# Performance work log

Measured on AMD Instinct MI355X. Metric: run time of the kernel, lower is better.

The kernel has to match this reference:

```python
import jax, jax.numpy as jnp
import numpy as np

EPS = 1e-5


def ste_sign(x):
    # Binarize(x) = sign(x) with straight-through identity gradient (torch .data trick)
    return x + jax.lax.stop_gradient(jnp.sign(x) - x)


def conv3x3(x, w):
    # NCHW 3x3 conv, stride 1, zero padding 1 (== ZeroPad2d(1) + 9 shifted views)
    return jax.lax.conv_general_dilated(x, w, (1, 1), [(1, 1), (1, 1)],
                                        dimension_numbers=('NCHW', 'OIHW', 'NCHW'))


def bconv(x, w):
    # Sum of 9 (or 18/36 channel-chunked) shifted binarized 1x1 convs == one binarized 3x3 conv.
    # sign(0)=0 on the zero padding, identical to padding the binarized input.
    return conv3x3(ste_sign(x), ste_sign(w))


def maxpool2(x):
    return jax.lax.reduce_window(x, -jnp.inf, jax.lax.max, (1, 1, 2, 2), (1, 1, 2, 2), 'VALID')


def bn(x, g, b):
    # eval-mode BatchNorm with fresh running stats (mean=0, var=1, eps=1e-5)
    scale = g * jax.lax.rsqrt(jnp.asarray(1.0 + EPS, x.dtype))
    shape = (1, -1) + (1,) * (x.ndim - 2)
    return x * scale.reshape(shape) + b.reshape(shape)


def htanh(x):
    return jnp.clip(x, -1.0, 1.0)


def blinear(x, w, b):
    # BinarizeLinear: in_features != 784 so both input and weight are binarized
    return ste_sign(x) @ ste_sign(w).T + b


def setup_inputs() -> dict:
    key = jax.random.key(0)
    ks = iter(jax.random.split(key, 48))

    def rn(shape, scale=0.05):
        return jax.random.normal(next(ks), shape, dtype=jnp.float32) * scale

    inp = {"x": jax.random.normal(next(ks), (128, 3, 32, 32), dtype=jnp.float32)}
    inp.update(
        w1=rn((128, 3, 3, 3)), c1b=rn((128,)),
        w2=rn((128, 128, 3, 3)),
        w3=rn((256, 128, 3, 3)),
        w4=rn((256, 256, 3, 3)),
        w5=rn((512, 256, 3, 3)),
        w6=rn((512, 512, 3, 3)),
        fw1=rn((1024, 8192)), fb1=rn((1024,)),
        fw2=rn((1024, 1024)), fb2=rn((1024,)),
        fw3=rn((10, 1024)), fb3=rn((10,)),
    )
    for name, c in [("1", 128), ("2", 128), ("3", 256), ("4", 256), ("5", 512), ("6", 512),
                    ("f1", 1024), ("f2", 1024), ("f3", 10)]:
        inp["g" + name] = jax.random.normal(next(ks), (c,), dtype=jnp.float32) * 0.1 + 1.0
        inp["bt" + name] = rn((c,))
    return inp


def reference(x, w1, c1b, w2, w3, w4, w5, w6,
              fw1, fb1, fw2, fb2, fw3, fb3,
              g1, bt1, g2, bt2, g3, bt3, g4, bt4, g5, bt5, g6, bt6,
              gf1, btf1, gf2, btf2, gf3, btf3):
    # block 1: first conv keeps the 3-channel input real, binarizes only the weight
    h = conv3x3(x, ste_sign(w1)) + c1b.reshape(1, -1, 1, 1)
    h = htanh(bn(h, g1, bt1))
    # block 2: 9 shifted binarized 1x1 convs (128->128) -> pool -> BN -> hardtanh
    h = htanh(bn(maxpool2(bconv(h, w2)), g2, bt2))
    # block 3: 9 convs 128->256
    h = htanh(bn(bconv(h, w3), g3, bt3))
    h = htanh(bn(maxpool2(bconv(h, w4)), g4, bt4))
    h = htanh(bn(bconv(h, w5), g5, bt5))
    h = htanh(bn(maxpool2(bconv(h, w6)), g6, bt6))
    h = h.reshape(h.shape[0], -1)  # [B, 512*4*4]
    h = htanh(bn(blinear(h, fw1, fb1), gf1, btf1))
    h = htanh(bn(blinear(h, fw2, fb2), gf2, btf2))
    h = bn(blinear(h, fw3, fb3), gf3, btf3)
    return jax.nn.log_softmax(h, axis=-1)
```

## Files before the change

### kernel.cpp

```cpp
#include <hip/hip_runtime.h>
#include <hip/hip_bf16.h>

using u32 = unsigned int;
using u64 = unsigned long long;
using s8  = signed char;
typedef int i32x4  __attribute__((ext_vector_type(4)));
typedef int i32x16 __attribute__((ext_vector_type(16)));

__device__ __forceinline__ s8 tsign(float t){
  return (t > 0.f) ? (s8)1 : ((t < 0.f) ? (s8)-1 : (s8)0);
}
__device__ __forceinline__ float bn_ts(float z, float sc, float b){
  return __fadd_rn(__fmul_rn(z, sc), b);
}

__global__ void scales_k(const float* g1, const float* g2, const float* g3,
                         const float* g4, const float* g5, const float* g6,
                         const float* gf1, const float* gf2, const float* gf3,
                         float* sc){
  int i = blockIdx.x*256 + threadIdx.x;
  const float rs = __fdiv_rn(1.0f, __fsqrt_rn((float)(1.0 + 1e-5)));
  float v;
  if      (i < 128)  v = g1[i];
  else if (i < 256)  v = g2[i-128];
  else if (i < 512)  v = g3[i-256];
  else if (i < 768)  v = g4[i-512];
  else if (i < 1280) v = g5[i-768];
  else if (i < 1792) v = g6[i-1280];
  else if (i < 2816) v = gf1[i-1792];
  else if (i < 3840) v = gf2[i-2816];
  else if (i < 3850) v = gf3[i-3840];
  else return;
  sc[i] = __fmul_rn(v, rs);
}

__global__ __launch_bounds__(256) void pack_wfrag_all_k(
    const float* __restrict__ w2, const float* __restrict__ w3,
    const float* __restrict__ w4, const float* __restrict__ w5,
    const float* __restrict__ w6,
    s8* __restrict__ wf2, s8* __restrict__ wf3, s8* __restrict__ wf4,
    s8* __restrict__ wf5, s8* __restrict__ wf6){
  int b = blockIdx.x;
  const float* w; s8* wf; int CIN, COUT, co;
  if      (b < 128) { w=w2; wf=wf2; CIN=128; COUT=128; co=b; }
  else if (b < 384) { w=w3; wf=wf3; CIN=128; COUT=256; co=b-128; }
  else if (b < 640) { w=w4; wf=wf4; CIN=256; COUT=256; co=b-384; }
  else if (b < 1152){ w=w5; wf=wf5; CIN=256; COUT=512; co=b-640; }
  else              { w=w6; wf=wf6; CIN=512; COUT=512; co=b-1152; }
  __shared__ s8 sb[4608];
  int nf = CIN*9;
  const float* wb = w + (size_t)co*nf;
  for (int i = threadIdx.x; i < nf; i += 256){
    float v = wb[i];
    sb[i] = (v > 0.f) ? (s8)1 : ((v < 0.f) ? (s8)-1 : (s8)0);
  }
  __syncthreads();
  int KK = CIN >> 5, CG = COUT >> 5;
  int cg = co >> 5, llo = co & 31;
  for (int i = threadIdx.x; i < nf; i += 256){
    int tap = i / CIN, k = i - tap*CIN;
    s8 v = sb[k*9 + tap];
    size_t dst = ((((size_t)tap*KK + (k>>5))*CG + cg)*64
                  + (llo + ((k>>4)&1)*32))*16 + (k&15);
    wf[dst] = v;
  }
}

__global__ void pack_w1_k(const float* __restrict__ w1, u32* __restrict__ wp1){
  int lane = threadIdx.x;
  bool hz = false;
  for (int h = 0; h < 2; h++){
    int co = h*64 + lane;
    u32 a = 0, s = 0, ctlw = 0;
    for (int tap = 0; tap < 9; tap++){
      float v0 = w1[(co*3 + 0)*9 + tap];
      float v1 = w1[(co*3 + 1)*9 + tap];
      float v2 = w1[(co*3 + 2)*9 + tap];
      int b0 = tap*3;
      a |= ((v0 != 0.f) ? 1u : 0u) << b0;     s |= ((v0 > 0.f) ? 1u : 0u) << b0;
      a |= ((v1 != 0.f) ? 1u : 0u) << (b0+1); s |= ((v1 > 0.f) ? 1u : 0u) << (b0+1);
      a |= ((v2 != 0.f) ? 1u : 0u) << (b0+2); s |= ((v2 > 0.f) ? 1u : 0u) << (b0+2);
      hz |= (v0 == 0.f) || (v1 == 0.f) || (v2 == 0.f);
      u32 f = (((v0 > 0.f) == (v1 > 0.f)) ? 1u : 0u)
            | ((v0 < 0.f) ? 2u : 0u)
            | ((v2 < 0.f) ? 4u : 0u);
      ctlw |= f << b0;
    }
    wp1[co*2]   = a;
    wp1[co*2+1] = s;
    wp1[256 + co] = ctlw;
  }
  u64 m = __ballot(hz);
  if (lane == 0) wp1[384] = (m != 0ull) ? 1u : 0u;
}

__global__ __launch_bounds__(256) void pack_fcB_k(const float* __restrict__ wa,
    const float* __restrict__ wb3, u32* __restrict__ wpa, u32* __restrict__ wpb){
  int b = blockIdx.x;
  const float* w; u32* wp; int COUT, co;
  if (b < 1024){ w = wa; wp = wpa; COUT = 1024; co = b; }
  else         { w = wb3; wp = wpb; COUT = 10;  co = b-1024; }
  __shared__ unsigned char sb[1024];
  const float* wbp = w + (size_t)co*1024;
  for (int i = threadIdx.x; i < 1024; i += 256){
    float v = wbp[i];
    sb[i] = (unsigned char)(((v != 0.f) ? 2u : 0u) | ((v > 0.f) ? 1u : 0u));
  }
  __syncthreads();
  for (int kw = threadIdx.x; kw < 32; kw += 256){
    u32 a = 0, s = 0;
    for (int j = 0; j < 32; j++){
      unsigned char bch = sb[kw*32 + j];
      a |= (u32)(bch >> 1) << j;
      s |= (u32)(bch & 1u) << j;
    }
    size_t o = ((size_t)kw*COUT + co)*2;
    wp[o] = a; wp[o+1] = s;
  }
}

__global__ __launch_bounds__(256) void pack_fc1_2k(const float* __restrict__ w,
    u32* __restrict__ wp){
  int co = blockIdx.x;
  __shared__ unsigned char sb[8192];
  const float* wb = w + (size_t)co*8192;
  for (int i = threadIdx.x; i < 8192; i += 256){
    float v = wb[i];
    sb[i] = (unsigned char)(((v != 0.f) ? 2u : 0u) | ((v > 0.f) ? 1u : 0u));
  }
  __syncthreads();
  int kw = threadIdx.x;
  int px = kw >> 4, cw = kw & 15;
  u32 a = 0, s = 0;
  for (int j = 0; j < 32; j++){
    unsigned char bch = sb[(cw*32 + j)*16 + px];
    a |= (u32)(bch >> 1) << j;
    s |= (u32)(bch & 1u) << j;
  }
  size_t o = ((size_t)kw*1024 + co)*2;
  wp[o] = a; wp[o+1] = s;
}

__global__ __launch_bounds__(256) void conv1_k(
    const float* __restrict__ x, const u32* __restrict__ wp1,
    const float* __restrict__ c1b,
    const float* __restrict__ sc1, const float* __restrict__ bt1,
    s8* __restrict__ s1){
  int tid = threadIdx.x, lane = tid & 63, wv = tid >> 6;
  int wid = blockIdx.x*4 + wv;
  int coh = wid & 1;
  int chunk = (wid >> 1) & 15;
  int n = wid >> 5;
  int py = lane >> 5, px = lane & 31;
  int y = chunk*2 + py;
  const float* xb = x + (size_t)n*3*1024;

  float xv[3][9];
  #pragma unroll
  for (int ci = 0; ci < 3; ci++)
    #pragma unroll
    for (int tap = 0; tap < 9; tap++){
      int yy = y + tap/3 - 1, xx = px + tap%3 - 1;
      bool ok = ((unsigned)yy < 32u) && ((unsigned)xx < 32u);
      xv[ci][tap] = ok ? xb[(ci*32 + yy)*32 + xx] : 0.f;
    }
  float pc0[9], pc1[9];
  #pragma unroll
  for (int tap = 0; tap < 9; tap++){
    pc0[tap] = __fadd_rn(xv[0][tap], xv[1][tap]);
    pc1[tap] = __fadd_rn(xv[0][tap], -xv[1][tap]);
  }

  size_t pixbase = (((size_t)n*1024) + y*32 + px)*128 + coh*64;
  bool fallback = (wp1[384] != 0u);

  if (!fallback){
    for (int co4 = 0; co4 < 64; co4 += 4){
      u32 outw = 0;
      #pragma unroll
      for (int j = 0; j < 4; j++){
        int co = coh*64 + co4 + j;
        u32 ctlw = wp1[256 + co];
        float acc = 0.f;
        #pragma unroll
        for (int tap = 0; tap < 9; tap++){
          u32 f = ctlw >> (3*tap);
          float s01 = (f & 1u) ? pc0[tap] : pc1[tap];
          s01 = __uint_as_float(__float_as_uint(s01) ^ ((f & 2u) << 30));
          float t2 = __uint_as_float(__float_as_uint(xv[2][tap]) ^ ((f & 4u) << 29));
          acc = __fadd_rn(acc, __fadd_rn(s01, t2));
        }
        float v = __fadd_rn(acc, c1b[co]);
        float t = bn_ts(v, sc1[co], bt1[co]);
        outw |= ((u32)(unsigned char)tsign(t)) << (8*j);
      }
      *reinterpret_cast<u32*>(&s1[pixbase + co4]) = outw;
    }
  } else {
    for (int co4 = 0; co4 < 64; co4 += 4){
      u32 outw = 0;
      #pragma unroll
      for (int j = 0; j < 4; j++){
        int co = coh*64 + co4 + j;
        u32 wA = wp1[co*2], wS = wp1[co*2+1];
        float acc = 0.f;
        #pragma unroll
        for (int tap = 0; tap < 9; tap++){
          float pt = 0.f;
          #pragma unroll
          for (int ci = 0; ci < 3; ci++){
            int bit = tap*3 + ci;
            float sg = ((wA >> bit) & 1u) ? (((wS >> bit) & 1u) ? 1.f : -1.f) : 0.f;
            pt = __fadd_rn(pt, __fmul_rn(sg, xv[ci][tap]));
          }
          acc = __fadd_rn(acc, pt);
        }
        float v = __fadd_rn(acc, c1b[co]);
        float t = bn_ts(v, sc1[co], bt1[co]);
        outw |= ((u32)(unsigned char)tsign(t)) << (8*j);
      }
      *reinterpret_cast<u32*>(&s1[pixbase + co4]) = outw;
    }
  }
}

template<int CIN, int COUT, int H, int W, int POOL, int BITOUT>
__global__ __launch_bounds__(256) void bconv_m(
    const s8* __restrict__ A, const s8* __restrict__ WF,
    const float* __restrict__ sc, const float* __restrict__ bt,
    s8* __restrict__ O, u32* __restrict__ OB){
  constexpr int KK = CIN/32, CG = COUT/32, CGB = 2;
  constexpr int XT = (W >= 16) ? 16 : 8;
  constexpr int YT = 32 / XT;
  constexpr int TPR = W / XT;
  constexpr int TROWS = H / YT;
  constexpr int HO = POOL ? H/2 : H, WO = POOL ? W/2 : W;
  int tid = threadIdx.x, lane = tid & 63, wv = tid >> 6;
  int wid = blockIdx.x*4 + wv;
  int cb = wid % (CG/CGB); int mt = wid / (CG/CGB);
  int tx = mt % TPR; int r0 = mt / TPR;
  int ty = r0 % TROWS; int n = r0 / TROWS;
  int y0 = ty*YT, x0 = tx*XT;
  int p = lane & 31;
  int py = p / XT, px = p % XT;
  int y = y0 + py, x = x0 + px;
  int kh = lane >> 5;
  const s8* An = A + (size_t)n*H*W*CIN;

  i32x16 acc0 = {0,0,0,0,0,0,0,0,0,0,0,0,0,0,0,0};
  i32x16 acc1 = {0,0,0,0,0,0,0,0,0,0,0,0,0,0,0,0};

  #pragma unroll
  for (int tap = 0; tap < 9; tap++){
    int dy = tap/3 - 1, dx = tap%3 - 1;
    int sy = y + dy, sx = x + dx;
    bool ok = ((unsigned)sy < (unsigned)H) && ((unsigned)sx < (unsigned)W);
    const s8* ap = An + ((size_t)sy*W + sx)*CIN + kh*16;
    const s8* wp = WF + (((size_t)tap*KK)*CG + (size_t)cb*CGB)*1024 + lane*16;
    #pragma unroll
    for (int kk = 0; kk < KK; kk++){
      i32x4 av = {0,0,0,0};
      if (ok) av = *reinterpret_cast<const i32x4*>(ap + kk*32);
      const s8* wk = wp + (size_t)kk*CG*1024;
      i32x4 b0 = *reinterpret_cast<const i32x4*>(wk);
      i32x4 b1 = *reinterpret_cast<const i32x4*>(wk + 1024);
      acc0 = __builtin_amdgcn_mfma_i32_32x32x32_i8(av, b0, acc0, 0, 0, 0);
      acc1 = __builtin_amdgcn_mfma_i32_32x32x32_i8(av, b1, acc1, 0, 0, 0);
    }
  }

  #pragma unroll
  for (int cgb = 0; cgb < CGB; cgb++){
    i32x16 acc = cgb ? acc1 : acc0;
    int co = (cb*CGB + cgb)*32 + (lane & 31);
    float ss = sc[co], bb = bt[co];
    if (POOL){
      constexpr int RY = (XT == 16) ? 8 : 4;
      #pragma unroll
      for (int q = 0; q < 4; q++){
        int rr = (q&1)*2 + (q>>1)*((XT == 16) ? 4 : 8);
        int z = max(max(acc[rr], acc[rr+1]), max(acc[rr+RY], acc[rr+RY+1]));
        float t = bn_ts((float)z, ss, bb);
        if (!BITOUT){
          int pb = (rr&3) + 8*(rr>>2) + 4*kh;
          int yy = y0 + pb/XT, xx2 = x0 + pb%XT;
          int oy = yy >> 1, ox = xx2 >> 1;
          O[(((size_t)n*HO + oy)*WO + ox)*COUT + co] = tsign(t);
        } else {
          u64 mP = __ballot(t > 0.f);
          u64 mN = __ballot(t < 0.f);
          if (lane == 0){
            u64 mA = mP | mN;
            int cw = cb*CGB + cgb;
            int pb0 = (rr&3) + 8*(rr>>2);
            int yy0 = y0 + pb0/XT, xx0 = x0 + pb0%XT;
            int p0 = (yy0>>1)*4 + (xx0>>1);
            int pb1 = pb0 + 4;
            int yy1 = y0 + pb1/XT, xx1 = x0 + pb1%XT;
            int p1 = (yy1>>1)*4 + (xx1>>1);
            size_t o0 = ((size_t)n*256 + p0*16 + cw)*2;
            size_t o1 = ((size_t)n*256 + p1*16 + cw)*2;
            OB[o0]   = (u32)mA;       OB[o0+1] = (u32)mP;
            OB[o1]   = (u32)(mA>>32); OB[o1+1] = (u32)(mP>>32);
          }
        }
      }
    } else {
      #pragma unroll
      for (int rr = 0; rr < 16; rr++){
        int pb = (rr&3) + 8*(rr>>2) + 4*kh;
        int yy = y0 + pb/XT, xx2 = x0 + pb%XT;
        float t = bn_ts((float)acc[rr], ss, bb);
        O[(((size_t)n*H + yy)*W + xx2)*COUT + co] = tsign(t);
      }
    }
  }
}

template<int KW>
__global__ __launch_bounds__(256) void fcb_k(
    const u32* __restrict__ A, const u32* __restrict__ Wp,
    const float* __restrict__ fb,
    const float* __restrict__ sc, const float* __restrict__ bt,
    u32* __restrict__ Op){
  int tid = threadIdx.x; int lane = tid & 63; int wv = tid >> 6;
  int wid = blockIdx.x*4 + wv;
  int og = wid & 15; int n = wid >> 4;
  int o = og*64 + lane;
  const uint2* a = reinterpret_cast<const uint2*>(&A[(size_t)n*KW*2]);
  int z = 0;
  #pragma unroll 8
  for (int kw = 0; kw < KW; kw++){
    uint2 av = a[kw];
    uint2 wv_ = reinterpret_cast<const uint2*>(Wp)[kw*1024 + o];
    u32 v = av.x & wv_.x;
    u32 d = v & (av.y ^ wv_.y);
    z += __popc(v) - 2*__popc(d);
  }
  float vv = __fadd_rn((float)z, fb[o]);
  float t = bn_ts(vv, sc[o], bt[o]);
  u64 mP = __ballot(t > 0.f);
  u64 mN = __ballot(t < 0.f);
  if (lane == 0){
    int ob = (n*32 + og*2)*2;
    Op[ob]   = (u32)(mP | mN);
    Op[ob+1] = (u32)mP;
    Op[ob+2] = (u32)((mP | mN) >> 32);
    Op[ob+3] = (u32)(mP >> 32);
  }
}

__global__ void fc3_k(const u32* __restrict__ A, const u32* __restrict__ Wp,
                      const float* __restrict__ fb,
                      const float* __restrict__ sc,
                      const float* __restrict__ bt,
                      float* __restrict__ out){
  int n = blockIdx.x; int lane = threadIdx.x;
  __shared__ double ls[10];
  double t = 0.0;
  if (lane < 10){
    const uint2* a = reinterpret_cast<const uint2*>(&A[(size_t)n*32*2]);
    int z = 0;
    for (int kw = 0; kw < 32; kw++){
      uint2 av = a[kw];
      uint2 wv_ = reinterpret_cast<const uint2*>(Wp)[kw*10 + lane];
      u32 v = av.x & wv_.x;
      u32 d = v & (av.y ^ wv_.y);
      z += __popc(v) - 2*__popc(d);
    }
    float vv = __fadd_rn((float)z, fb[lane]);
    float tf = bn_ts(vv, sc[lane], bt[lane]);
    t = (double)tf;
    ls[lane] = t;
  }
  __syncthreads();
  if (lane < 10){
    double m = -1e300;
    for (int j = 0; j < 10; j++) m = fmax(m, ls[j]);
    double sum = 0.0;
    for (int j = 0; j < 10; j++) sum += exp(ls[j] - m);
    double r = t - m - log(sum);
    out[n*10 + lane] = (float)r;
  }
}

extern "C" void kernel_launch(void* const* d_in, const int* in_sizes, int n_in,
                              void* d_out, int out_size, void* d_ws, size_t ws_size,
                              hipStream_t stream){
  auto f = [&](int i){ return (const float*)d_in[i]; };
  const float *x  = f(0),  *w1 = f(1),  *c1b = f(2),
    *w2 = f(3),  *w3 = f(4),  *w4 = f(5),  *w5 = f(6),  *w6 = f(7),
    *fw1 = f(8), *fb1 = f(9), *fw2 = f(10), *fb2 = f(11),
    *fw3 = f(12), *fb3 = f(13),
    *g1 = f(14), *bt1 = f(15), *g2 = f(16), *bt2 = f(17),
    *g3 = f(18), *bt3 = f(19), *g4 = f(20), *bt4 = f(21),
    *g5 = f(22), *bt5 = f(23), *g6 = f(24), *bt6 = f(25),
    *gf1 = f(26), *btf1 = f(27), *gf2 = f(28), *btf2 = f(29),
    *gf3 = f(30), *btf3 = f(31);

  char* base = (char*)d_ws;
  size_t off = 0;
  auto alloc = [&](size_t bytes){ char* p = base + off; off += (bytes + 255) & ~(size_t)255; return p; };
  s8* poolA = (s8*)alloc(128ull*32*32*128);
  s8* poolB = (s8*)alloc(128ull*16*16*128);
  s8 *s1 = poolA, *s3 = poolA, *s5 = poolA;
  s8 *s2 = poolB, *s4 = poolB;
  s8 *wf2 = (s8*)alloc(9ull*128*128), *wf3 = (s8*)alloc(9ull*128*256),
     *wf4 = (s8*)alloc(9ull*256*256), *wf5 = (s8*)alloc(9ull*256*512),
     *wf6 = (s8*)alloc(9ull*512*512);
  u32 *wp1  = (u32*)alloc(385*4);
  float* scb = (float*)alloc(3850*4);
  u32 *fw1p = (u32*)alloc(2ull*256*1024*4), *fw2p = (u32*)alloc(2ull*32*1024*4),
      *fw3p = (u32*)alloc(2ull*32*10*4);
  u32 *s6p  = (u32*)alloc(2ull*128*256*4);
  u32 *sf1  = (u32*)alloc(2ull*128*32*4), *sf2 = (u32*)alloc(2ull*128*32*4);

  float *sc1 = scb, *sc2 = scb+128, *sc3 = scb+256, *sc4 = scb+512,
        *sc5 = scb+768, *sc6 = scb+1280, *scf1 = scb+1792, *scf2 = scb+2816,
        *scf3 = scb+3840;

  scales_k<<<16, 256, 0, stream>>>(g1,g2,g3,g4,g5,g6,gf1,gf2,gf3, scb);
  pack_w1_k<<<1, 64, 0, stream>>>(w1, wp1);
  pack_wfrag_all_k<<<1664, 256, 0, stream>>>(w2,w3,w4,w5,w6, wf2,wf3,wf4,wf5,wf6);
  pack_fc1_2k<<<1024, 256, 0, stream>>>(fw1, fw1p);
  pack_fcB_k<<<1034, 256, 0, stream>>>(fw2, fw3, fw2p, fw3p);

  conv1_k<<<1024, 256, 0, stream>>>(x, wp1, c1b, sc1, bt1, s1);
  bconv_m<128,128,32,32,1,0><<<2048, 256, 0, stream>>>(s1, wf2, sc2, bt2, s2, nullptr);
  bconv_m<128,256,16,16,0,0><<<1024, 256, 0, stream>>>(s2, wf3, sc3, bt3, s3, nullptr);
  bconv_m<256,256,16,16,1,0><<<1024, 256, 0, stream>>>(s3, wf4, sc4, bt4, s4, nullptr);
  bconv_m<256,512, 8, 8,0,0><<< 512, 256, 0, stream>>>(s4, wf5, sc5, bt5, s5, nullptr);
  bconv_m<512,512, 8, 8,1,1><<< 512, 256, 0, stream>>>(s5, wf6, sc6, bt6, nullptr, s6p);
  fcb_k<256><<<(128*16)/4, 256, 0, stream>>>(s6p, fw1p, fb1, scf1, btf1, sf1);
  fcb_k<32><<<(128*16)/4,  256, 0, stream>>>(sf1, fw2p, fb2, scf2, btf2, sf2);
  fc3_k<<<128, 64, 0, stream>>>(sf2, fw3p, fb3, scf3, btf3, (float*)d_out);
}
```

Baseline: 352.2 us.

## Widen bconv wave tile to four output groups and split conv1 channels finer

Each bconv wave now computes 128 output channels (four MFMA accumulators) per 32-pixel tile instead of 64, so every activation load is reused across twice as many output channels. The work mapping is also reordered so consecutive waves share a channel group and walk over pixel tiles, improving weight locality, and grid sizes are halved to match. conv1 splits output channels into four quarters per pixel, doubling its grid, and stages results in registers so it writes two 16-byte stores instead of many 4-byte ones. The wider tile raises register pressure and gives fewer waves for small layers, which may lower occupancy.

```diff
diff --git a/kernel.cpp b/kernel.cpp
--- a/kernel.cpp
+++ b/kernel.cpp
@@ -148,9 +148,9 @@
     s8* __restrict__ s1){
   int tid = threadIdx.x, lane = tid & 63, wv = tid >> 6;
   int wid = blockIdx.x*4 + wv;
-  int coh = wid & 1;
-  int chunk = (wid >> 1) & 15;
-  int n = wid >> 5;
+  int coh = wid & 3;
+  int chunk = (wid >> 2) & 15;
+  int n = wid >> 6;
   int py = lane >> 5, px = lane & 31;
   int y = chunk*2 + py;
   const float* xb = x + (size_t)n*3*1024;
@@ -171,15 +171,17 @@
     pc1[tap] = __fadd_rn(xv[0][tap], -xv[1][tap]);
   }
 
-  size_t pixbase = (((size_t)n*1024) + y*32 + px)*128 + coh*64;
+  size_t pixbase = (((size_t)n*1024) + y*32 + px)*128 + coh*32;
   bool fallback = (wp1[384] != 0u);
+  u32 ow[8];
 
   if (!fallback){
-    for (int co4 = 0; co4 < 64; co4 += 4){
+    #pragma unroll
+    for (int co4 = 0; co4 < 32; co4 += 4){
       u32 outw = 0;
       #pragma unroll
       for (int j = 0; j < 4; j++){
-        int co = coh*64 + co4 + j;
+        int co = coh*32 + co4 + j;
         u32 ctlw = wp1[256 + co];
         float acc = 0.f;
         #pragma unroll
@@ -194,14 +196,15 @@
         float t = bn_ts(v, sc1[co], bt1[co]);
         outw |= ((u32)(unsigned char)tsign(t)) << (8*j);
       }
-      *reinterpret_cast<u32*>(&s1[pixbase + co4]) = outw;
+      ow[co4/4] = outw;
     }
   } else {
-    for (int co4 = 0; co4 < 64; co4 += 4){
+    #pragma unroll
+    for (int co4 = 0; co4 < 32; co4 += 4){
       u32 outw = 0;
       #pragma unroll
       for (int j = 0; j < 4; j++){
-        int co = coh*64 + co4 + j;
+        int co = coh*32 + co4 + j;
         u32 wA = wp1[co*2], wS = wp1[co*2+1];
         float acc = 0.f;
         #pragma unroll
@@ -219,9 +222,13 @@
         float t = bn_ts(v, sc1[co], bt1[co]);
         outw |= ((u32)(unsigned char)tsign(t)) << (8*j);
       }
-      *reinterpret_cast<u32*>(&s1[pixbase + co4]) = outw;
-    }
-  }
+      ow[co4/4] = outw;
+    }
+  }
+  uint4 st0 = { ow[0], ow[1], ow[2], ow[3] };
+  uint4 st1 = { ow[4], ow[5], ow[6], ow[7] };
+  *reinterpret_cast<uint4*>(&s1[pixbase])      = st0;
+  *reinterpret_cast<uint4*>(&s1[pixbase + 16]) = st1;
 }
 
 template<int CIN, int COUT, int H, int W, int POOL, int BITOUT>
@@ -229,15 +236,17 @@
     const s8* __restrict__ A, const s8* __restrict__ WF,
     const float* __restrict__ sc, const float* __restrict__ bt,
     s8* __restrict__ O, u32* __restrict__ OB){
-  constexpr int KK = CIN/32, CG = COUT/32, CGB = 2;
+  constexpr int KK = CIN/32, CG = COUT/32;
   constexpr int XT = (W >= 16) ? 16 : 8;
   constexpr int YT = 32 / XT;
   constexpr int TPR = W / XT;
   constexpr int TROWS = H / YT;
+  constexpr int NMT = 128*TROWS*TPR;
   constexpr int HO = POOL ? H/2 : H, WO = POOL ? W/2 : W;
+  constexpr int RY = (XT == 16) ? 8 : 4;
   int tid = threadIdx.x, lane = tid & 63, wv = tid >> 6;
   int wid = blockIdx.x*4 + wv;
-  int cb = wid % (CG/CGB); int mt = wid / (CG/CGB);
+  int mt = wid % NMT; int cb = wid / NMT;
   int tx = mt % TPR; int r0 = mt / TPR;
   int ty = r0 % TROWS; int n = r0 / TROWS;
   int y0 = ty*YT, x0 = tx*XT;
@@ -248,7 +257,7 @@
   const s8* An = A + (size_t)n*H*W*CIN;
 
   i32x16 acc0 = {0,0,0,0,0,0,0,0,0,0,0,0,0,0,0,0};
-  i32x16 acc1 = {0,0,0,0,0,0,0,0,0,0,0,0,0,0,0,0};
+  i32x16 acc1 = acc0, acc2 = acc0, acc3 = acc0;
 
   #pragma unroll
   for (int tap = 0; tap < 9; tap++){
@@ -256,7 +265,7 @@
     int sy = y + dy, sx = x + dx;
     bool ok = ((unsigned)sy < (unsigned)H) && ((unsigned)sx < (unsigned)W);
     const s8* ap = An + ((size_t)sy*W + sx)*CIN + kh*16;
-    const s8* wp = WF + (((size_t)tap*KK)*CG + (size_t)cb*CGB)*1024 + lane*16;
+    const s8* wp = WF + (((size_t)tap*KK)*CG + (size_t)cb*4)*1024 + lane*16;
     #pragma unroll
     for (int kk = 0; kk < KK; kk++){
       i32x4 av = {0,0,0,0};
@@ -264,18 +273,19 @@
       const s8* wk = wp + (size_t)kk*CG*1024;
       i32x4 b0 = *reinterpret_cast<const i32x4*>(wk);
       i32x4 b1 = *reinterpret_cast<const i32x4*>(wk + 1024);
+      i32x4 b2 = *reinterpret_cast<const i32x4*>(wk + 2048);
+      i32x4 b3 = *reinterpret_cast<const i32x4*>(wk + 3072);
       acc0 = __builtin_amdgcn_mfma_i32_32x32x32_i8(av, b0, acc0, 0, 0, 0);
       acc1 = __builtin_amdgcn_mfma_i32_32x32x32_i8(av, b1, acc1, 0, 0, 0);
-    }
-  }
-
-  #pragma unroll
-  for (int cgb = 0; cgb < CGB; cgb++){
-    i32x16 acc = cgb ? acc1 : acc0;
-    int co = (cb*CGB + cgb)*32 + (lane & 31);
+      acc2 = __builtin_amdgcn_mfma_i32_32x32x32_i8(av, b2, acc2, 0, 0, 0);
+      acc3 = __builtin_amdgcn_mfma_i32_32x32x32_i8(av, b3, acc3, 0, 0, 0);
+    }
+  }
+
+  auto epi = [&](const i32x16& acc, int cgb){
+    int co = (cb*4 + cgb)*32 + (lane & 31);
     float ss = sc[co], bb = bt[co];
     if (POOL){
-      constexpr int RY = (XT == 16) ? 8 : 4;
       #pragma unroll
       for (int q = 0; q < 4; q++){
         int rr = (q&1)*2 + (q>>1)*((XT == 16) ? 4 : 8);
@@ -291,7 +301,7 @@
           u64 mN = __ballot(t < 0.f);
           if (lane == 0){
             u64 mA = mP | mN;
-            int cw = cb*CGB + cgb;
+            int cw = cb*4 + cgb;
             int pb0 = (rr&3) + 8*(rr>>2);
             int yy0 = y0 + pb0/XT, xx0 = x0 + pb0%XT;
             int p0 = (yy0>>1)*4 + (xx0>>1);
@@ -314,7 +324,8 @@
         O[(((size_t)n*H + yy)*W + xx2)*COUT + co] = tsign(t);
       }
     }
-  }
+  };
+  epi(acc0, 0); epi(acc1, 1); epi(acc2, 2); epi(acc3, 3);
 }
 
 template<int KW>
@@ -425,12 +436,12 @@
   pack_fc1_2k<<<1024, 256, 0, stream>>>(fw1, fw1p);
   pack_fcB_k<<<1034, 256, 0, stream>>>(fw2, fw3, fw2p, fw3p);
 
-  conv1_k<<<1024, 256, 0, stream>>>(x, wp1, c1b, sc1, bt1, s1);
-  bconv_m<128,128,32,32,1,0><<<2048, 256, 0, stream>>>(s1, wf2, sc2, bt2, s2, nullptr);
-  bconv_m<128,256,16,16,0,0><<<1024, 256, 0, stream>>>(s2, wf3, sc3, bt3, s3, nullptr);
-  bconv_m<256,256,16,16,1,0><<<1024, 256, 0, stream>>>(s3, wf4, sc4, bt4, s4, nullptr);
-  bconv_m<256,512, 8, 8,0,0><<< 512, 256, 0, stream>>>(s4, wf5, sc5, bt5, s5, nullptr);
-  bconv_m<512,512, 8, 8,1,1><<< 512, 256, 0, stream>>>(s5, wf6, sc6, bt6, nullptr, s6p);
+  conv1_k<<<2048, 256, 0, stream>>>(x, wp1, c1b, sc1, bt1, s1);
+  bconv_m<128,128,32,32,1,0><<<1024, 256, 0, stream>>>(s1, wf2, sc2, bt2, s2, nullptr);
+  bconv_m<128,256,16,16,0,0><<< 512, 256, 0, stream>>>(s2, wf3, sc3, bt3, s3, nullptr);
+  bconv_m<256,256,16,16,1,0><<< 512, 256, 0, stream>>>(s3, wf4, sc4, bt4, s4, nullptr);
+  bconv_m<256,512, 8, 8,0,0><<< 256, 256, 0, stream>>>(s4, wf5, sc5, bt5, s5, nullptr);
+  bconv_m<512,512, 8, 8,1,1><<< 256, 256, 0, stream>>>(s5, wf6, sc6, bt6, nullptr, s6p);
   fcb_k<256><<<(128*16)/4, 256, 0, stream>>>(s6p, fw1p, fb1, scf1, btf1, sf1);
   fcb_k<32><<<(128*16)/4,  256, 0, stream>>>(sf1, fw2p, fb2, scf2, btf2, sf2);
   fc3_k<<<128, 64, 0, stream>>>(sf2, fw3p, fb3, scf3, btf3, (float*)d_out);
```

Measured after the change: 389.5 us. 1.11x slower.
